# Performance work log

Measured on AMD Instinct MI355X. Metric: run time of the kernel, lower is better.

## Reference

```python
import jax, jax.numpy as jnp
import numpy as np

K = 1000   # grid rows (detections from model 1, truncated to 1000)
N = 1000   # grid cols (detections from model 2)
M = 900000 # number of non-empty (overlapping) pairs
F = 7      # per-pair feature dim
SENTINEL = -9999.0


def setup_inputs() -> dict:
    key = jax.random.key(0)
    ks = jax.random.split(key, 12)
    def w(k, o, i):
        return jax.random.normal(k, (o, i), dtype=jnp.float32) * 0.05
    def b(k, o):
        return jax.random.normal(k, (o,), dtype=jnp.float32) * 0.05
    return {
        "input_1": jax.random.normal(ks[0], (1, F, 1, M), dtype=jnp.float32),
        "T_out": jnp.zeros((1, K, N), dtype=jnp.float32),
        "T_indices": jax.random.randint(ks[1], (2, M), 0, K),
        "w1": w(ks[2], 18, F),  "b1": b(ks[3], 18),
        "w2": w(ks[4], 36, 18), "b2": b(ks[5], 36),
        "w3": w(ks[6], 36, 36), "b3": b(ks[7], 36),
        "w4": w(ks[8], 1, 36),  "b4": b(ks[9], 1),
    }


def reference(input_1, T_out, T_indices, w1, b1, w2, b2, w3, b3, w4, b4):
    # 1x1 conv stack == channel matmuls on the flattened [F, M] features.
    x = input_1[0, :, 0, :]                       # [F, M]
    h = jax.nn.relu(w1 @ x + b1[:, None])         # [18, M]
    h = jax.nn.relu(w2 @ h + b2[:, None])         # [36, M]
    h = jax.nn.relu(w3 @ h + b3[:, None])         # [36, M]
    vals = (w4 @ h + b4[:, None])[0]              # [M]

    grid = jnp.full(T_out.shape, SENTINEL, dtype=T_out.dtype)  # [1, K, N]
    grid = grid.at[:, T_indices[0], T_indices[1]].set(vals[None, :])

    # MaxPool2d([1, N]) -> max over cols; MaxPool2d([K, 1]) -> max over rows.
    row_max = grid.max(axis=2).squeeze()          # [K]
    col_max = grid.max(axis=1).squeeze()          # [N]
    return (row_max, col_max)
```

## Files before the change

### kernel.cpp

```cpp
#include <hip/hip_runtime.h>
#include <stdint.h>

#define KK 1000
#define NN 1000
#define MM 900000
#define FF 7
#define SENTINEL -9999.0f

typedef __fp16 f16x8 __attribute__((ext_vector_type(8)));
typedef float  f32x4 __attribute__((ext_vector_type(4)));

template <int N, typename F>
__device__ __forceinline__ void unroll_loop(F&& f) {
    if constexpr (N > 0) {
        unroll_loop<N - 1>(static_cast<F&&>(f));
        f(N - 1);
    }
}

__device__ __forceinline__ unsigned pk2(float a, float b) {
    return __builtin_bit_cast(unsigned, __builtin_amdgcn_cvt_pkrtz(a, b));
}

#define ZB ((KK * NN / 2 + 255) / 256)
#define SB 4

__global__ __launch_bounds__(256) void prep(ulonglong2* __restrict__ g,
                                            float* __restrict__ outcol) {
    int b = blockIdx.x;
    if (b < ZB) {
        int i = b * 256 + threadIdx.x;
        if (i < KK * NN / 2) g[i] = make_ulonglong2(0ULL, 0ULL);
    } else {
        int i = (b - ZB) * 256 + threadIdx.x;
        if (i < NN) outcol[i] = SENTINEL;
    }
}

#define W2_OFF  0
#define W3_OFF  3840
#define W4_OFF  10752
#define B2_OFF  10944
#define B3_OFF  11136
#define ACT_OFF 11328
#define LDS_BYTES (ACT_OFF + 4 * 9216)

__global__ __launch_bounds__(256, 3) void mlp_scatter(
    const float* __restrict__ in,
    const int*   __restrict__ idx,
    const float* __restrict__ w1, const float* __restrict__ b1,
    const float* __restrict__ w2, const float* __restrict__ b2,
    const float* __restrict__ w3, const float* __restrict__ b3,
    const float* __restrict__ w4, const float* __restrict__ b4,
    unsigned long long* __restrict__ grid)
{
    __shared__ __align__(16) char smem[LDS_BYTES];
    const int t = threadIdx.x;

    for (int i = t; i < LDS_BYTES / 16; i += 256)
        ((uint4*)smem)[i] = make_uint4(0, 0, 0, 0);
    __syncthreads();

    for (int i = t; i < 36 * 18; i += 256) {
        int r = i / 18, k = i - r * 18;
        ((__fp16*)(smem + W2_OFF + r * 80))[k] = (__fp16)w2[i];
    }
    for (int i = t; i < 36 * 36; i += 256) {
        int r = i / 36, k = i - r * 36;
        ((__fp16*)(smem + W3_OFF + r * 144))[k] = (__fp16)w3[i];
    }
    if (t < 36) {
        ((float*)(smem + W4_OFF))[t] = w4[t];
        ((float*)(smem + B2_OFF))[t] = b2[t];
        ((float*)(smem + B3_OFF))[t] = b3[t];
    }
    __syncthreads();

    const int wave = t >> 6, l = t & 63;
    const int g = l >> 4, li = l & 15;
    char* act = smem + ACT_OFF + wave * 9216;
    const int mbase = blockIdx.x * 256 + wave * 64;
    if (mbase >= MM) return;

    const int m = mbase + l;
    const int mc = m < MM ? m : MM - 1;
    float x[FF];
    unroll_loop<FF>([&](int f) { x[f] = in[(size_t)f * MM + mc]; });

    unsigned hw[9];
    unroll_loop<9>([&](int p) {
        float a = b1[2 * p], b = b1[2 * p + 1];
        unroll_loop<FF>([&](int i) {
            a = fmaf(w1[(2 * p) * FF + i], x[i], a);
            b = fmaf(w1[(2 * p + 1) * FF + i], x[i], b);
        });
        hw[p] = pk2(fmaxf(a, 0.0f), fmaxf(b, 0.0f));
    });
    {
        char* row = act + l * 144;
        *(uint4*)(row)      = make_uint4(hw[0], hw[1], hw[2], hw[3]);
        *(uint4*)(row + 16) = make_uint4(hw[4], hw[5], hw[6], hw[7]);
        *(uint2*)(row + 32) = make_uint2(hw[8], 0u);
    }

    const f32x4 zf = {0.f, 0.f, 0.f, 0.f};

    f16x8 a2[3], bq[4];
    unroll_loop<3>([&](int T) {
        a2[T] = *(const f16x8*)(smem + W2_OFF + (16 * T + li) * 80 + g * 16);
    });
    unroll_loop<4>([&](int q) {
        bq[q] = *(const f16x8*)(act + (16 * q + li) * 144 + g * 16);
    });
    f32x4 b2v[3];
    unroll_loop<3>([&](int T) {
        b2v[T] = *(const f32x4*)(smem + B2_OFF + (16 * T + 4 * g) * 4);
    });
    f32x4 acc[3][4];
    unroll_loop<3>([&](int T) { unroll_loop<4>([&](int q) {
        acc[T][q] = __builtin_amdgcn_mfma_f32_16x16x32_f16(a2[T], bq[q], zf, 0, 0, 0);
    }); });
    unroll_loop<3>([&](int T) { unroll_loop<4>([&](int q) {
        f32x4 d = acc[T][q];
        unsigned lo = pk2(fmaxf(d[0] + b2v[T][0], 0.0f), fmaxf(d[1] + b2v[T][1], 0.0f));
        unsigned hi = pk2(fmaxf(d[2] + b2v[T][2], 0.0f), fmaxf(d[3] + b2v[T][3], 0.0f));
        *(uint2*)(act + (16 * q + li) * 144 + (16 * T + 4 * g) * 2) = make_uint2(lo, hi);
    }); });

    f16x8 a3[3][2];
    unroll_loop<3>([&](int T) { unroll_loop<2>([&](int s) {
        a3[T][s] = *(const f16x8*)(smem + W3_OFF + (16 * T + li) * 144 + s * 64 + g * 16);
    }); });
    f32x4 wv[3], b3v[3];
    unroll_loop<3>([&](int T) {
        wv[T]  = *(const f32x4*)(smem + W4_OFF + (16 * T + 4 * g) * 4);
        b3v[T] = *(const f32x4*)(smem + B3_OFF + (16 * T + 4 * g) * 4);
    });
    float vfin = 0.0f;
    unroll_loop<4>([&](int q) {
        const char* brow = act + (16 * q + li) * 144;
        f16x8 bb0 = *(const f16x8*)(brow + g * 16);
        f16x8 bb1 = *(const f16x8*)(brow + 64 + g * 16);
        float s = 0.0f;
        unroll_loop<3>([&](int T) {
            f32x4 c = __builtin_amdgcn_mfma_f32_16x16x32_f16(a3[T][0], bb0, zf, 0, 0, 0);
            c = __builtin_amdgcn_mfma_f32_16x16x32_f16(a3[T][1], bb1, c, 0, 0, 0);
            s += wv[T][0] * fmaxf(c[0] + b3v[T][0], 0.0f)
               + wv[T][1] * fmaxf(c[1] + b3v[T][1], 0.0f)
               + wv[T][2] * fmaxf(c[2] + b3v[T][2], 0.0f)
               + wv[T][3] * fmaxf(c[3] + b3v[T][3], 0.0f);
        });
        s += __shfl_xor(s, 16);
        s += __shfl_xor(s, 32);
        if (g == q) vfin = s;
    });

    const int mf = mbase + 16 * g + li;
    if (mf < MM) {
        float v = vfin + b4[0];
        int r = idx[mf];
        int c = idx[MM + mf];
        unsigned long long packed =
            ((unsigned long long)(unsigned)(mf + 1) << 32) | (unsigned)__float_as_uint(v);
        atomicMax(&grid[r * NN + c], packed);
    }
}

#define CCH 50
#define CR  (KK / CCH)

__global__ __launch_bounds__(256) void maxes(const unsigned long long* __restrict__ g,
                                             float* __restrict__ out) {
    int b = blockIdx.x;
    if (b < KK) {
        int r = b;
        float mx = SENTINEL;
        for (int c = threadIdx.x; c < NN; c += 256) {
            unsigned long long p = g[(size_t)r * NN + c];
            if (p) mx = fmaxf(mx, __uint_as_float((unsigned)p));
        }
        __shared__ float red[256];
        red[threadIdx.x] = mx;
        __syncthreads();
        for (int s = 128; s > 0; s >>= 1) {
            if (threadIdx.x < s)
                red[threadIdx.x] = fmaxf(red[threadIdx.x], red[threadIdx.x + s]);
            __syncthreads();
        }
        if (threadIdx.x == 0) out[r] = red[0];
    } else {
        int cb = b - KK;
        int n  = (cb & 3) * 256 + (int)threadIdx.x;
        if (n < NN) {
            int k0 = (cb >> 2) * CR;
            float mx = SENTINEL;
            for (int k = k0; k < k0 + CR; ++k) {
                unsigned long long p = g[(size_t)k * NN + n];
                if (p) mx = fmaxf(mx, __uint_as_float((unsigned)p));
            }
            atomicMax(out + KK + n, mx);
        }
    }
}

extern "C" void kernel_launch(void* const* d_in, const int* in_sizes, int n_in,
                              void* d_out, int out_size, void* d_ws, size_t ws_size,
                              hipStream_t stream) {
    const float* in  = (const float*)d_in[0];
    const int*   idx = (const int*)d_in[2];
    const float* w1  = (const float*)d_in[3];
    const float* b1  = (const float*)d_in[4];
    const float* w2  = (const float*)d_in[5];
    const float* b2  = (const float*)d_in[6];
    const float* w3  = (const float*)d_in[7];
    const float* b3  = (const float*)d_in[8];
    const float* w4  = (const float*)d_in[9];
    const float* b4  = (const float*)d_in[10];

    unsigned long long* grid = (unsigned long long*)d_ws;
    float* out = (float*)d_out;

    prep<<<ZB + SB, 256, 0, stream>>>((ulonglong2*)grid, out + KK);

    mlp_scatter<<<(MM + 255) / 256, 256, 0, stream>>>(
        in, idx, w1, b1, w2, b2, w3, b3, w4, b4, grid);

    maxes<<<KK + 4 * CCH, 256, 0, stream>>>(grid, out);
}
```

Baseline: 159.6 us.

## Make MLP kernel persistent and shrink per-wave LDS activation buffers

```diff
diff --git a/kernel.cpp b/kernel.cpp
--- a/kernel.cpp
+++ b/kernel.cpp
@@ -37,15 +37,15 @@
     }
 }
 
-#define W2_OFF  0
-#define W3_OFF  3840
-#define W4_OFF  10752
-#define B2_OFF  10944
-#define B3_OFF  11136
-#define ACT_OFF 11328
-#define LDS_BYTES (ACT_OFF + 4 * 9216)
-
-__global__ __launch_bounds__(256, 3) void mlp_scatter(
+#define W2_OFF   0
+#define W3_OFF   3840
+#define WGT_BYTES 10752
+#define H2_OFF   5120
+#define WAVE_ACT 7424
+#define LDS_BYTES (WGT_BYTES + 4 * WAVE_ACT)
+#define GRID_BLKS 1024
+
+__global__ __launch_bounds__(256, 4) void mlp_scatter(
     const float* __restrict__ in,
     const int*   __restrict__ idx,
     const float* __restrict__ w1, const float* __restrict__ b1,
@@ -56,11 +56,26 @@
 {
     __shared__ __align__(16) char smem[LDS_BYTES];
     const int t = threadIdx.x;
-
-    for (int i = t; i < LDS_BYTES / 16; i += 256)
+    const int wave = t >> 6, l = t & 63;
+    const int g = l >> 4, li = l & 15;
+    char* hs1 = smem + WGT_BYTES + wave * WAVE_ACT;
+    char* hs2 = hs1 + H2_OFF;
+
+    for (int i = t; i < WGT_BYTES / 16; i += 256)
         ((uint4*)smem)[i] = make_uint4(0, 0, 0, 0);
+    {
+        char* row = hs1 + l * 80;
+        *(uint2*)(row + 40) = make_uint2(0, 0);
+        *(uint4*)(row + 48) = make_uint4(0, 0, 0, 0);
+        *(uint4*)(row + 64) = make_uint4(0, 0, 0, 0);
+    }
+    if (l < 16) {
+        char* row = hs2 + l * 144;
+        *(uint4*)(row + 96)  = make_uint4(0, 0, 0, 0);
+        *(uint4*)(row + 112) = make_uint4(0, 0, 0, 0);
+        *(uint4*)(row + 128) = make_uint4(0, 0, 0, 0);
+    }
     __syncthreads();
-
     for (int i = t; i < 36 * 18; i += 256) {
         int r = i / 18, k = i - r * 18;
         ((__fp16*)(smem + W2_OFF + r * 80))[k] = (__fp16)w2[i];
@@ -69,100 +84,85 @@
         int r = i / 36, k = i - r * 36;
         ((__fp16*)(smem + W3_OFF + r * 144))[k] = (__fp16)w3[i];
     }
-    if (t < 36) {
-        ((float*)(smem + W4_OFF))[t] = w4[t];
-        ((float*)(smem + B2_OFF))[t] = b2[t];
-        ((float*)(smem + B3_OFF))[t] = b3[t];
-    }
     __syncthreads();
 
-    const int wave = t >> 6, l = t & 63;
-    const int g = l >> 4, li = l & 15;
-    char* act = smem + ACT_OFF + wave * 9216;
-    const int mbase = blockIdx.x * 256 + wave * 64;
-    if (mbase >= MM) return;
-
-    const int m = mbase + l;
-    const int mc = m < MM ? m : MM - 1;
-    float x[FF];
-    unroll_loop<FF>([&](int f) { x[f] = in[(size_t)f * MM + mc]; });
-
-    unsigned hw[9];
-    unroll_loop<9>([&](int p) {
-        float a = b1[2 * p], b = b1[2 * p + 1];
-        unroll_loop<FF>([&](int i) {
-            a = fmaf(w1[(2 * p) * FF + i], x[i], a);
-            b = fmaf(w1[(2 * p + 1) * FF + i], x[i], b);
+    const f32x4 zf = {0.f, 0.f, 0.f, 0.f};
+    f16x8 a2[3], a3[3][2];
+    f32x4 b2v[3], b3v[3], wv[3];
+    unroll_loop<3>([&](int T) {
+        a2[T]    = *(const f16x8*)(smem + W2_OFF + (16 * T + li) * 80 + g * 16);
+        a3[T][0] = *(const f16x8*)(smem + W3_OFF + (16 * T + li) * 144 + g * 16);
+        a3[T][1] = *(const f16x8*)(smem + W3_OFF + (16 * T + li) * 144 + 64 + g * 16);
+        int r0 = 16 * T + 4 * g;
+        b2v[T] = r0 < 36 ? *(const f32x4*)(b2 + r0) : zf;
+        b3v[T] = r0 < 36 ? *(const f32x4*)(b3 + r0) : zf;
+        wv[T]  = r0 < 36 ? *(const f32x4*)(w4 + r0) : zf;
+    });
+    const float fb4 = b4[0];
+
+    for (int tile = blockIdx.x; tile * 256 < MM; tile += GRID_BLKS) {
+        const int mbase = tile * 256 + wave * 64;
+        const int m  = mbase + l;
+        const int mc = m < MM ? m : MM - 1;
+
+        float x[FF];
+        unroll_loop<FF>([&](int f) { x[f] = in[(size_t)f * MM + mc]; });
+        unsigned hw[9];
+        unroll_loop<9>([&](int p) {
+            float a = b1[2 * p], b = b1[2 * p + 1];
+            unroll_loop<FF>([&](int i) {
+                a = fmaf(w1[(2 * p) * FF + i], x[i], a);
+                b = fmaf(w1[(2 * p + 1) * FF + i], x[i], b);
+            });
+            hw[p] = pk2(fmaxf(a, 0.0f), fmaxf(b, 0.0f));
         });
-        hw[p] = pk2(fmaxf(a, 0.0f), fmaxf(b, 0.0f));
-    });
-    {
-        char* row = act + l * 144;
-        *(uint4*)(row)      = make_uint4(hw[0], hw[1], hw[2], hw[3]);
-        *(uint4*)(row + 16) = make_uint4(hw[4], hw[5], hw[6], hw[7]);
-        *(uint2*)(row + 32) = make_uint2(hw[8], 0u);
-    }
-
-    const f32x4 zf = {0.f, 0.f, 0.f, 0.f};
-
-    f16x8 a2[3], bq[4];
-    unroll_loop<3>([&](int T) {
-        a2[T] = *(const f16x8*)(smem + W2_OFF + (16 * T + li) * 80 + g * 16);
-    });
-    unroll_loop<4>([&](int q) {
-        bq[q] = *(const f16x8*)(act + (16 * q + li) * 144 + g * 16);
-    });
-    f32x4 b2v[3];
-    unroll_loop<3>([&](int T) {
-        b2v[T] = *(const f32x4*)(smem + B2_OFF + (16 * T + 4 * g) * 4);
-    });
-    f32x4 acc[3][4];
-    unroll_loop<3>([&](int T) { unroll_loop<4>([&](int q) {
-        acc[T][q] = __builtin_amdgcn_mfma_f32_16x16x32_f16(a2[T], bq[q], zf, 0, 0, 0);
-    }); });
-    unroll_loop<3>([&](int T) { unroll_loop<4>([&](int q) {
-        f32x4 d = acc[T][q];
-        unsigned lo = pk2(fmaxf(d[0] + b2v[T][0], 0.0f), fmaxf(d[1] + b2v[T][1], 0.0f));
-        unsigned hi = pk2(fmaxf(d[2] + b2v[T][2], 0.0f), fmaxf(d[3] + b2v[T][3], 0.0f));
-        *(uint2*)(act + (16 * q + li) * 144 + (16 * T + 4 * g) * 2) = make_uint2(lo, hi);
-    }); });
-
-    f16x8 a3[3][2];
-    unroll_loop<3>([&](int T) { unroll_loop<2>([&](int s) {
-        a3[T][s] = *(const f16x8*)(smem + W3_OFF + (16 * T + li) * 144 + s * 64 + g * 16);
-    }); });
-    f32x4 wv[3], b3v[3];
-    unroll_loop<3>([&](int T) {
-        wv[T]  = *(const f32x4*)(smem + W4_OFF + (16 * T + 4 * g) * 4);
-        b3v[T] = *(const f32x4*)(smem + B3_OFF + (16 * T + 4 * g) * 4);
-    });
-    float vfin = 0.0f;
-    unroll_loop<4>([&](int q) {
-        const char* brow = act + (16 * q + li) * 144;
-        f16x8 bb0 = *(const f16x8*)(brow + g * 16);
-        f16x8 bb1 = *(const f16x8*)(brow + 64 + g * 16);
-        float s = 0.0f;
-        unroll_loop<3>([&](int T) {
-            f32x4 c = __builtin_amdgcn_mfma_f32_16x16x32_f16(a3[T][0], bb0, zf, 0, 0, 0);
-            c = __builtin_amdgcn_mfma_f32_16x16x32_f16(a3[T][1], bb1, c, 0, 0, 0);
-            s += wv[T][0] * fmaxf(c[0] + b3v[T][0], 0.0f)
-               + wv[T][1] * fmaxf(c[1] + b3v[T][1], 0.0f)
-               + wv[T][2] * fmaxf(c[2] + b3v[T][2], 0.0f)
-               + wv[T][3] * fmaxf(c[3] + b3v[T][3], 0.0f);
+        {
+            char* row = hs1 + l * 80;
+            *(uint4*)(row)      = make_uint4(hw[0], hw[1], hw[2], hw[3]);
+            *(uint4*)(row + 16) = make_uint4(hw[4], hw[5], hw[6], hw[7]);
+            *(uint2*)(row + 32) = make_uint2(hw[8], 0u);
+        }
+
+        float vfin = 0.0f;
+        unroll_loop<4>([&](int q) {
+            f16x8 bq = *(const f16x8*)(hs1 + (16 * q + li) * 80 + g * 16);
+            f32x4 acc[3];
+            unroll_loop<3>([&](int T) {
+                acc[T] = __builtin_amdgcn_mfma_f32_16x16x32_f16(a2[T], bq, zf, 0, 0, 0);
+            });
+            unroll_loop<3>([&](int T) {
+                unsigned lo = pk2(fmaxf(acc[T][0] + b2v[T][0], 0.0f),
+                                  fmaxf(acc[T][1] + b2v[T][1], 0.0f));
+                unsigned hi = pk2(fmaxf(acc[T][2] + b2v[T][2], 0.0f),
+                                  fmaxf(acc[T][3] + b2v[T][3], 0.0f));
+                *(uint2*)(hs2 + li * 144 + (16 * T + 4 * g) * 2) = make_uint2(lo, hi);
+            });
+            f16x8 bb0 = *(const f16x8*)(hs2 + li * 144 + g * 16);
+            f16x8 bb1 = *(const f16x8*)(hs2 + li * 144 + 64 + g * 16);
+            float s = 0.0f;
+            unroll_loop<3>([&](int T) {
+                f32x4 c = __builtin_amdgcn_mfma_f32_16x16x32_f16(a3[T][0], bb0, zf, 0, 0, 0);
+                c = __builtin_amdgcn_mfma_f32_16x16x32_f16(a3[T][1], bb1, c, 0, 0, 0);
+                s += wv[T][0] * fmaxf(c[0] + b3v[T][0], 0.0f)
+                   + wv[T][1] * fmaxf(c[1] + b3v[T][1], 0.0f)
+                   + wv[T][2] * fmaxf(c[2] + b3v[T][2], 0.0f)
+                   + wv[T][3] * fmaxf(c[3] + b3v[T][3], 0.0f);
+            });
+            s += __shfl_xor(s, 16);
+            s += __shfl_xor(s, 32);
+            if (g == q) vfin = s;
         });
-        s += __shfl_xor(s, 16);
-        s += __shfl_xor(s, 32);
-        if (g == q) vfin = s;
-    });
-
-    const int mf = mbase + 16 * g + li;
-    if (mf < MM) {
-        float v = vfin + b4[0];
-        int r = idx[mf];
-        int c = idx[MM + mf];
-        unsigned long long packed =
-            ((unsigned long long)(unsigned)(mf + 1) << 32) | (unsigned)__float_as_uint(v);
-        atomicMax(&grid[r * NN + c], packed);
+
+        const int mf = mbase + 16 * g + li;
+        if (mf < MM) {
+            float v = vfin + fb4;
+            int r = idx[mf];
+            int c = idx[MM + mf];
+            unsigned long long packed =
+                ((unsigned long long)(unsigned)(mf + 1) << 32) |
+                (unsigned)__float_as_uint(v);
+            atomicMax(&grid[r * NN + c], packed);
+        }
     }
 }
 
@@ -222,7 +222,7 @@
 
     prep<<<ZB + SB, 256, 0, stream>>>((ulonglong2*)grid, out + KK);
 
-    mlp_scatter<<<(MM + 255) / 256, 256, 0, stream>>>(
+    mlp_scatter<<<GRID_BLKS, 256, 0, stream>>>(
         in, idx, w1, b1, w2, b2, w3, b3, w4, b4, grid);
 
     maxes<<<KK + 4 * CCH, 256, 0, stream>>>(grid, out);
```

Result: faster. 151.9 us (-4.8%).
